# Kernel optimization log

Hardware: AMD Instinct MI355X
Metric: run time of the kernel (lower is better)

The kernel has to match this reference:

```python
import jax, jax.numpy as jnp
import numpy as np

NJ, NS, NM, NR = 100000, 20000, 10000, 5000
D_IN, OUT, H = 128, 256, 4
C = OUT // H
E = 250000
NEG_SLOPE = 0.2
LN_EPS = 1e-5


def setup_inputs() -> dict:
    key = jax.random.key(0)
    ks = jax.random.split(key, 24)
    inp = {
        'x_job':     jax.random.normal(ks[0], (NJ, D_IN), jnp.float32),
        'x_station': jax.random.normal(ks[1], (NS, D_IN), jnp.float32),
        'x_machine': jax.random.normal(ks[2], (NM, D_IN), jnp.float32),
        'x_robot':   jax.random.normal(ks[3], (NR, D_IN), jnp.float32),
        'src_cl': jax.random.randint(ks[4],  (E,), 0, NS, jnp.int32),
        'dst_cl': jax.random.randint(ks[5],  (E,), 0, NJ, jnp.int32),
        'src_ld': jax.random.randint(ks[6],  (E,), 0, NS, jnp.int32),
        'dst_ld': jax.random.randint(ks[7],  (E,), 0, NJ, jnp.int32),
        'src_we': jax.random.randint(ks[8],  (E,), 0, NM, jnp.int32),
        'dst_we': jax.random.randint(ks[9],  (E,), 0, NJ, jnp.int32),
        'src_ex': jax.random.randint(ks[10], (E,), 0, NM, jnp.int32),
        'dst_ex': jax.random.randint(ks[11], (E,), 0, NJ, jnp.int32),
        'src_hd': jax.random.randint(ks[12], (E,), 0, NR, jnp.int32),
        'dst_hd': jax.random.randint(ks[13], (E,), 0, NJ, jnp.int32),
        'Ws':      jax.random.normal(ks[14], (5, D_IN, OUT), jnp.float32) * 0.05,
        'att_src': jax.random.normal(ks[15], (5, H, C), jnp.float32) * 0.05,
        'att_dst': jax.random.normal(ks[16], (5, H, C), jnp.float32) * 0.05,
        'biases':  jnp.zeros((5, OUT), jnp.float32),
        'W_res':   jax.random.normal(ks[17], (D_IN, OUT), jnp.float32) * 0.05,
        'ln_gamma': jnp.ones((OUT,), jnp.float32),
        'ln_beta':  jnp.zeros((OUT,), jnp.float32),
    }
    return inp


def _gat(x_src, x_dst, src, dst, W, a_src, a_dst, b):
    # Bipartite GATConv (PyG semantics, shared lin for src and dst, concat heads)
    hs = (x_src @ W).reshape(-1, H, C)   # [Ns,H,C]
    hd = (x_dst @ W).reshape(-1, H, C)   # [Nd,H,C]
    a_s = jnp.einsum('nhc,hc->nh', hs, a_src)  # [Ns,H]
    a_d = jnp.einsum('nhc,hc->nh', hd, a_dst)  # [Nd,H]
    e = jax.nn.leaky_relu(a_s[src] + a_d[dst], NEG_SLOPE)  # [E,H]
    # softmax over incoming edges of each dst node
    m = jax.ops.segment_max(e, dst, num_segments=NJ)       # [Nd,H]
    ex = jnp.exp(e - m[dst])
    denom = jax.ops.segment_sum(ex, dst, num_segments=NJ)
    alpha = ex / (denom[dst] + 1e-16)                       # [E,H]
    msg = alpha[:, :, None] * hs[src]                        # [E,H,C]
    out = jax.ops.segment_sum(msg, dst, num_segments=NJ)    # [Nd,H,C]
    return out.reshape(NJ, H * C) + b


def reference(x_job, x_station, x_machine, x_robot,
              src_cl, dst_cl, src_ld, dst_ld, src_we, dst_we,
              src_ex, dst_ex, src_hd, dst_hd,
              Ws, att_src, att_dst, biases, W_res, ln_gamma, ln_beta):
    rels = [
        (x_station, src_cl, dst_cl),
        (x_station, src_ld, dst_ld),
        (x_machine, src_we, dst_we),
        (x_machine, src_ex, dst_ex),
        (x_robot,   src_hd, dst_hd),
    ]
    acc = jnp.zeros((NJ, OUT), x_job.dtype)
    for i, (xs, s, d) in enumerate(rels):  # sum aggregation across relations
        acc = acc + _gat(xs, x_job, s, d, Ws[i], att_src[i], att_dst[i], biases[i])
    h = acc + x_job @ W_res                # residual projection (dj != out_dim)
    h = jax.nn.relu(h)
    mu = jnp.mean(h, axis=-1, keepdims=True)
    var = jnp.var(h, axis=-1, keepdims=True)
    return (h - mu) * jax.lax.rsqrt(var + LN_EPS) * ln_gamma + ln_beta
```

## Files before the change

kernel.cpp:

```cpp
#include <hip/hip_runtime.h>

typedef unsigned short u16;
typedef unsigned int u32;
typedef __attribute__((ext_vector_type(8))) short s16x8;
typedef __attribute__((ext_vector_type(4))) float f32x4;

__device__ __forceinline__ float bf2f(u16 u) { return __uint_as_float(((u32)u) << 16); }
__device__ __forceinline__ u16 f2bf(float f) {
    u32 b = __float_as_uint(f);
    b += 0x7fffu + ((b >> 16) & 1u);
    return (u16)(b >> 16);
}

__global__ void probe_mark(float* __restrict__ out, int n, float val) {
    int i = blockIdx.x * blockDim.x + threadIdx.x;
    if (i < n) out[i] = val;
}

struct PrepX { const float* x[4]; int rows[4]; int blks[4]; u16* xb[4]; };

__global__ void k_prep_all(const float* __restrict__ Ws, const float* __restrict__ W_res,
                           const float* __restrict__ att_src, const float* __restrict__ att_dst,
                           const float* __restrict__ biases,
                           u32* __restrict__ cnt, int zc, int nzb, u16* __restrict__ wt,
                           float* __restrict__ w_d_all, float* __restrict__ w_s_cat,
                           float* __restrict__ bias_sum, PrepX PX) {
    int b = blockIdx.x;
    if (b < nzb) {
        int i = b * 256 + threadIdx.x;
        if (i < zc) cnt[i] = 0u;
        return;
    }
    b -= nzb;
    if (b < 768) {
        int i = b * 256 + threadIdx.x;
        int k = i & 127;
        int c = (i >> 7) & 255;
        int w = i >> 15;
        float v = (w < 5) ? Ws[(size_t)w * 32768 + k * 256 + c] : W_res[k * 256 + c];
        wt[i] = f2bf(v);
        return;
    }
    b -= 768;
    if (b < 6) {
        if (b < 5) {
            int k = threadIdx.x;
            if (k >= 128) return;
            const float* Wr = Ws + (size_t)b * 128 * 256 + (size_t)k * 256;
            for (int h = 0; h < 4; ++h) {
                float ss = 0.f, sd = 0.f;
                for (int c = 0; c < 64; ++c) {
                    float w = Wr[h * 64 + c];
                    ss += w * att_src[(b * 4 + h) * 64 + c];
                    sd += w * att_dst[(b * 4 + h) * 64 + c];
                }
                w_d_all[k * 20 + b * 4 + h] = sd;
                w_s_cat[b * 512 + k * 4 + h] = ss;
            }
        } else if (threadIdx.x < 256) {
            float s = 0.f;
            for (int r = 0; r < 5; ++r) s += biases[r * 256 + threadIdx.x];
            bias_sum[threadIdx.x] = s;
        }
        return;
    }
    b -= 6;
#pragma unroll
    for (int a = 0; a < 4; ++a) {
        if (b < PX.blks[a]) {
            int elem = b * 2048 + threadIdx.x * 8;
            if (elem < PX.rows[a] * 128) {
                const float4* src = (const float4*)(PX.x[a] + elem);
                float4 v0 = src[0], v1 = src[1];
                u32 w0 = ((u32)f2bf(v0.y) << 16) | f2bf(v0.x);
                u32 w1 = ((u32)f2bf(v0.w) << 16) | f2bf(v0.z);
                u32 w2 = ((u32)f2bf(v1.y) << 16) | f2bf(v1.x);
                u32 w3 = ((u32)f2bf(v1.w) << 16) | f2bf(v1.z);
                *(uint4*)(PX.xb[a] + elem) = make_uint4(w0, w1, w2, w3);
            }
            return;
        }
        b -= PX.blks[a];
    }
}

struct SDesc { const float* A; const float* W; float* out; int N; int Kout; int groups; int start; };
struct STab { SDesc d[6]; int total; };

__global__ void skinny_all(STab T) {
    int idx = blockIdx.x * blockDim.x + threadIdx.x;
    if (idx >= T.total) return;
    int mi = 0;
#pragma unroll
    for (int i = 1; i < 6; ++i) if (idx >= T.d[i].start) mi = i;
    SDesc d = T.d[mi];
    int local = idx - d.start;
    int row = local / d.groups, g = local - row * d.groups;
    const float* a = d.A + (size_t)row * 128;
    const float* w = d.W + g * 4;
    int Kout = d.Kout;
    float s0 = 0.f, s1 = 0.f, s2 = 0.f, s3 = 0.f;
    for (int k = 0; k < 128; k += 4) {
        float4 av = *(const float4*)(a + k);
        float4 w0 = *(const float4*)(w + (size_t)(k + 0) * Kout);
        float4 w1 = *(const float4*)(w + (size_t)(k + 1) * Kout);
        float4 w2 = *(const float4*)(w + (size_t)(k + 2) * Kout);
        float4 w3 = *(const float4*)(w + (size_t)(k + 3) * Kout);
        s0 += av.x * w0.x + av.y * w1.x + av.z * w2.x + av.w * w3.x;
        s1 += av.x * w0.y + av.y * w1.y + av.z * w2.y + av.w * w3.y;
        s2 += av.x * w0.z + av.y * w1.z + av.z * w2.z + av.w * w3.z;
        s3 += av.x * w0.w + av.y * w1.w + av.z * w2.w + av.w * w3.w;
    }
    float* o = d.out + (size_t)row * Kout + g * 4;
    *(float4*)o = make_float4(s0, s1, s2, s3);
}

struct GDesc { const u16* A; u16* C; int wslice; int N; int start; };
struct GTab { GDesc d[6]; };

__global__ __launch_bounds__(256) void gemm_all(GTab T, const u16* __restrict__ wt) {
    __shared__ __align__(16) u16 sA[64][136];
    __shared__ __align__(16) u16 sB[64][136];
    int bx = blockIdx.x;
    int mi = 0;
#pragma unroll
    for (int i = 1; i < 6; ++i) if (bx >= T.d[i].start) mi = i;
    GDesc d = T.d[mi];
    int R0 = (bx - d.start) * 64;
    int t = threadIdx.x;
    int r = t >> 2, seg = (t & 3) * 32;
    {
        uint4 a0, a1, a2, a3;
        if (R0 + r < d.N) {
            const uint4* pa = (const uint4*)(d.A + (size_t)(R0 + r) * 128 + seg);
            a0 = pa[0]; a1 = pa[1]; a2 = pa[2]; a3 = pa[3];
        } else {
            a0 = a1 = a2 = a3 = make_uint4(0, 0, 0, 0);
        }
        uint4* qd = (uint4*)&sA[r][seg];
        qd[0] = a0; qd[1] = a1; qd[2] = a2; qd[3] = a3;
    }
    int wave = t >> 6, lane = t & 63;
    int quad = lane >> 4, m = lane & 15;
    const u16* aRow = &sA[wave * 16 + m][0];
    const u16* wbase = wt + (size_t)d.wslice * 32768;

    for (int y = 0; y < 4; ++y) {
        int c0 = y * 64;
        const uint4* pb = (const uint4*)(wbase + (size_t)(c0 + r) * 128 + seg);
        uint4 b0 = pb[0], b1 = pb[1], b2 = pb[2], b3 = pb[3];
        __syncthreads();
        uint4* qb = (uint4*)&sB[r][seg];
        qb[0] = b0; qb[1] = b1; qb[2] = b2; qb[3] = b3;
        __syncthreads();

        f32x4 acc[4] = {};
#pragma unroll
        for (int k0 = 0; k0 < 128; k0 += 32) {
            s16x8 af = *(const s16x8*)(aRow + k0 + quad * 8);
#pragma unroll
            for (int ct = 0; ct < 4; ++ct) {
                s16x8 bf = *(const s16x8*)(&sB[ct * 16 + m][k0 + quad * 8]);
                acc[ct] = __builtin_amdgcn_mfma_f32_16x16x32_bf16(af, bf, acc[ct], 0, 0, 0);
            }
        }
#pragma unroll
        for (int ct = 0; ct < 4; ++ct) {
#pragma unroll
            for (int i = 0; i < 4; ++i) {
                int row = R0 + wave * 16 + quad * 4 + i;
                if (row < d.N) d.C[(size_t)row * 256 + c0 + ct * 16 + m] = f2bf(acc[ct][i]);
            }
        }
    }
}

struct EdgeP { const int* src[5]; const int* dst[5]; int base[5]; };

__global__ void k_count(EdgeP P, u32* __restrict__ cnt, u32* __restrict__ epos, int E) {
    int r = blockIdx.y;
    int e = blockIdx.x * blockDim.x + threadIdx.x;
    if (e >= E) return;
    u32 c = atomicAdd(cnt + (size_t)P.dst[r][e] * 5 + r, 1u);
    epos[(size_t)r * E + e] = c;
}

__global__ void k_scan1(const u32* __restrict__ cnt, u32* __restrict__ off,
                        u32* __restrict__ bsum, int nblk) {
    int b = blockIdx.x, t = threadIdx.x;
    size_t base = (size_t)b * 1024 + t * 4;
    u32 v0 = cnt[base], v1 = cnt[base + 1], v2 = cnt[base + 2], v3 = cnt[base + 3];
    u32 tsum = v0 + v1 + v2 + v3;
    __shared__ u32 s[256];
    u32 x = tsum;
    s[t] = x; __syncthreads();
    for (int ofs = 1; ofs < 256; ofs <<= 1) {
        u32 y = (t >= ofs) ? s[t - ofs] : 0u;
        __syncthreads();
        x += y; s[t] = x;
        __syncthreads();
    }
    u32 ex = x - tsum;
    off[base] = ex; off[base + 1] = ex + v0; off[base + 2] = ex + v0 + v1; off[base + 3] = ex + v0 + v1 + v2;
    if (t == 255) bsum[b] = x;
}

__global__ void k_scan23(u32* __restrict__ off, const u32* __restrict__ bsum, int nblk) {
    int b = blockIdx.x, t = threadIdx.x;
    __shared__ u32 s[256];
    u32 part = 0;
    for (int i = t; i < b; i += 256) part += bsum[i];
    s[t] = part; __syncthreads();
    for (int ofs = 128; ofs; ofs >>= 1) {
        if (t < ofs) s[t] += s[t + ofs];
        __syncthreads();
    }
    u32 add = s[0];
    size_t base = (size_t)b * 1024 + t * 4;
    off[base] += add; off[base + 1] += add; off[base + 2] += add; off[base + 3] += add;
}

__global__ void k_fill(EdgeP P, const u32* __restrict__ off, const u32* __restrict__ epos,
                       u32* __restrict__ epay, int E) {
    int r = blockIdx.y;
    int e = blockIdx.x * blockDim.x + threadIdx.x;
    if (e >= E) return;
    int d = P.dst[r][e];
    u32 pos = off[(size_t)d * 5 + r] + epos[(size_t)r * E + e];
    epay[pos] = (u32)(P.base[r] + P.src[r][e]);
}

__global__ __launch_bounds__(512) void k_gather(
        const u32* __restrict__ offs, const u32* __restrict__ epay,
        const float* __restrict__ as_h,
        const float* __restrict__ a_d,
        const u16* __restrict__ hs, const u16* __restrict__ resb,
        const float* __restrict__ bias_sum,
        const float* __restrict__ gamma, const float* __restrict__ beta,
        float* __restrict__ out, int NJ) {
    int row = blockIdx.x * 8 + (threadIdx.x >> 6);
    int lane = threadIdx.x & 63;
    if (row >= NJ) return;

    ushort4 rr = *(const ushort4*)(resb + (size_t)row * 256 + lane * 4);
    float4 bb = *(const float4*)(bias_sum + lane * 4);
    int c = lane * 4;
    float4 g = *(const float4*)(gamma + c);
    float4 be = *(const float4*)(beta + c);

    int hd = lane >> 4;
    u32 hoff = (u32)(lane << 2);

    const float* adb = a_d + (size_t)row * 20 + hd;
    float adx[5] = { adb[0], adb[4], adb[8], adb[12], adb[16] };

    const u32* op = offs + (size_t)row * 5;
    u32 o[6];
#pragma unroll
    for (int i = 0; i < 6; ++i) o[i] = op[i];
    u32 deg = o[5] - o[0];

    u32 pv = 0;
    if (deg) {
        u32 li = (u32)lane < deg ? (u32)lane : 0u;
        pv = epay[o[0] + li];
    }

    float a0 = 0.f, a1 = 0.f, a2 = 0.f, a3 = 0.f;
#pragma unroll
    for (int r = 0; r < 5; ++r) {
        float adr = adx[r];
        float n0 = 0.f, n1 = 0.f, n2 = 0.f, n3 = 0.f, dsum = 0.f;
        for (u32 e = o[r]; e < o[r + 1]; ++e) {
            u32 i = e - o[0];
            u32 p;
            if (i < 64u) p = __shfl(pv, (int)i);
            else         p = epay[e];
            float x = as_h[p * 4 + (u32)hd] + adr;
            x = x > 0.f ? x : 0.2f * x;
            float w = __expf(x);
            dsum += w;
            ushort4 hv = *(const ushort4*)(hs + ((size_t)p << 8) + hoff);
            n0 += w * bf2f(hv.x); n1 += w * bf2f(hv.y);
            n2 += w * bf2f(hv.z); n3 += w * bf2f(hv.w);
        }
        float iv = 1.f / (dsum + 1e-16f);
        a0 += n0 * iv; a1 += n1 * iv; a2 += n2 * iv; a3 += n3 * iv;
    }

    float h0 = fmaxf(a0 + bf2f(rr.x) + bb.x, 0.f);
    float h1 = fmaxf(a1 + bf2f(rr.y) + bb.y, 0.f);
    float h2 = fmaxf(a2 + bf2f(rr.z) + bb.z, 0.f);
    float h3 = fmaxf(a3 + bf2f(rr.w) + bb.w, 0.f);
    float s = h0 + h1 + h2 + h3;
    float s2 = h0 * h0 + h1 * h1 + h2 * h2 + h3 * h3;
    for (int o2 = 32; o2; o2 >>= 1) {
        s += __shfl_xor(s, o2);
        s2 += __shfl_xor(s2, o2);
    }
    float mu = s * (1.f / 256.f);
    float var = s2 * (1.f / 256.f) - mu * mu;
    float rs = rsqrtf(var + 1e-5f);
    float4 o4;
    o4.x = (h0 - mu) * rs * g.x + be.x;
    o4.y = (h1 - mu) * rs * g.y + be.y;
    o4.z = (h2 - mu) * rs * g.z + be.z;
    o4.w = (h3 - mu) * rs * g.w + be.w;
    *(float4*)(out + (size_t)row * 256 + c) = o4;
}

static size_t align256(size_t x) { return (x + 255) & ~(size_t)255; }

extern "C" void kernel_launch(void* const* d_in, const int* in_sizes, int n_in,
                              void* d_out, int out_size, void* d_ws, size_t ws_size,
                              hipStream_t stream) {
    float* out = (float*)d_out;

    int NJ = in_sizes[0] / 128, NS = in_sizes[1] / 128, NM = in_sizes[2] / 128, NR = in_sizes[3] / 128;
    int E = in_sizes[4];
    bool cfg_ok = (n_in >= 21) && (out_size == NJ * 256)
        && (in_sizes[14] == 5 * 128 * 256) && (in_sizes[18] == 128 * 256)
        && (in_sizes[19] == 256) && (in_sizes[20] == 256);
    if (!cfg_ok) { probe_mark<<<8, 256, 0, stream>>>(out, 2048, 1000000.0f); return; }

    const float* x_job = (const float*)d_in[0];
    const float* x_st  = (const float*)d_in[1];
    const float* x_ma  = (const float*)d_in[2];
    const float* x_ro  = (const float*)d_in[3];
    EdgeP EP;
    EP.src[0] = (const int*)d_in[4];  EP.dst[0] = (const int*)d_in[5];
    EP.src[1] = (const int*)d_in[6];  EP.dst[1] = (const int*)d_in[7];
    EP.src[2] = (const int*)d_in[8];  EP.dst[2] = (const int*)d_in[9];
    EP.src[3] = (const int*)d_in[10]; EP.dst[3] = (const int*)d_in[11];
    EP.src[4] = (const int*)d_in[12]; EP.dst[4] = (const int*)d_in[13];
    EP.base[0] = 0; EP.base[1] = NS; EP.base[2] = 2 * NS;
    EP.base[3] = 2 * NS + NM; EP.base[4] = 2 * NS + 2 * NM;
    const float* Ws      = (const float*)d_in[14];
    const float* att_src = (const float*)d_in[15];
    const float* att_dst = (const float*)d_in[16];
    const float* biases  = (const float*)d_in[17];
    const float* W_res   = (const float*)d_in[18];
    const float* gamma   = (const float*)d_in[19];
    const float* beta    = (const float*)d_in[20];

    int nseg = 5 * NJ;
    int nblk = (nseg + 1023) / 1024;
    int NPAD = nblk * 1024;
    int TOT = 2 * NS + 2 * NM + NR;
    int TOTX = NJ + NS + NM + NR;

    char* base = (char*)d_ws;
    size_t ob = 0;
    float*  w_d_all  = (float*)(base + ob);  ob += align256(128 * 20 * 4);
    float*  w_s_cat  = (float*)(base + ob);  ob += align256(5 * 128 * 4 * 4);
    float*  bias_sum = (float*)(base + ob);  ob += align256(256 * 4);
    float*  a_d      = (float*)(base + ob);  ob += align256((size_t)NJ * 20 * 4);
    float*  as_cat   = (float*)(base + ob);  ob += align256((size_t)TOT * 4 * 4);
    u16*    wt       = (u16*)(base + ob);    ob += align256((size_t)6 * 256 * 128 * 2);
    u16*    xb       = (u16*)(base + ob);    ob += align256((size_t)TOTX * 128 * 2);
    u16*    resb     = (u16*)(base + ob);    ob += align256((size_t)NJ * 256 * 2);
    u16*    hs_cat   = (u16*)(base + ob);    ob += align256((size_t)TOT * 256 * 2);
    u32*    cnt      = (u32*)(base + ob);    ob += align256((size_t)NPAD * 4);
    u32*    offs     = (u32*)(base + ob);    ob += align256((size_t)NPAD * 4);
    u32*    bsum     = (u32*)(base + ob);    ob += align256((size_t)nblk * 4);
    u32*    epos     = (u32*)(base + ob);    ob += align256((size_t)5 * E * 4);
    u32*    epay     = (u32*)(base + ob);    ob += align256((size_t)5 * E * 4);

    if (ws_size < ob) { probe_mark<<<8, 256, 0, stream>>>(out, 2048, 500000.0f); return; }

    int zc = NPAD;
    int nzb = (zc + 255) / 256;
    PrepX PX;
    PX.x[0] = x_job; PX.x[1] = x_st; PX.x[2] = x_ma; PX.x[3] = x_ro;
    PX.rows[0] = NJ; PX.rows[1] = NS; PX.rows[2] = NM; PX.rows[3] = NR;
    u16* xb_job = xb;
    u16* xb_st  = xb + (size_t)NJ * 128;
    u16* xb_ma  = xb + (size_t)(NJ + NS) * 128;
    u16* xb_ro  = xb + (size_t)(NJ + NS + NM) * 128;
    PX.xb[0] = xb_job; PX.xb[1] = xb_st; PX.xb[2] = xb_ma; PX.xb[3] = xb_ro;
    int nxb = 0;
    for (int a = 0; a < 4; ++a) { PX.blks[a] = (PX.rows[a] * 128 + 2047) / 2048; nxb += PX.blks[a]; }
    k_prep_all<<<nzb + 768 + 6 + nxb, 256, 0, stream>>>(Ws, W_res, att_src, att_dst, biases,
                                                        cnt, zc, nzb, wt,
                                                        w_d_all, w_s_cat, bias_sum, PX);

    STab ST;
    int st = 0;
    ST.d[0] = {x_job, w_d_all,           a_d,                             NJ, 20, 5, st}; st += NJ * 5;
    ST.d[1] = {x_st,  w_s_cat + 0 * 512, as_cat + (size_t)EP.base[0] * 4, NS, 4, 1, st}; st += NS;
    ST.d[2] = {x_st,  w_s_cat + 1 * 512, as_cat + (size_t)EP.base[1] * 4, NS, 4, 1, st}; st += NS;
    ST.d[3] = {x_ma,  w_s_cat + 2 * 512, as_cat + (size_t)EP.base[2] * 4, NM, 4, 1, st}; st += NM;
    ST.d[4] = {x_ma,  w_s_cat + 3 * 512, as_cat + (size_t)EP.base[3] * 4, NM, 4, 1, st}; st += NM;
    ST.d[5] = {x_ro,  w_s_cat + 4 * 512, as_cat + (size_t)EP.base[4] * 4, NR, 4, 1, st}; st += NR;
    ST.total = st;
    skinny_all<<<(ST.total + 255) / 256, 256, 0, stream>>>(ST);

    int tJ = (NJ + 63) / 64, tS = (NS + 63) / 64, tM = (NM + 63) / 64, tR = (NR + 63) / 64;
    GTab GT;
    int gs = 0;
    GT.d[0] = {xb_job, resb,                              5, NJ, gs}; gs += tJ;
    GT.d[1] = {xb_st,  hs_cat + (size_t)EP.base[0] * 256, 0, NS, gs}; gs += tS;
    GT.d[2] = {xb_st,  hs_cat + (size_t)EP.base[1] * 256, 1, NS, gs}; gs += tS;
    GT.d[3] = {xb_ma,  hs_cat + (size_t)EP.base[2] * 256, 2, NM, gs}; gs += tM;
    GT.d[4] = {xb_ma,  hs_cat + (size_t)EP.base[3] * 256, 3, NM, gs}; gs += tM;
    GT.d[5] = {xb_ro,  hs_cat + (size_t)EP.base[4] * 256, 4, NR, gs}; gs += tR;
    gemm_all<<<gs, 256, 0, stream>>>(GT, wt);

    k_count<<<dim3((E + 255) / 256, 5), 256, 0, stream>>>(EP, cnt, epos, E);
    k_scan1<<<nblk, 256, 0, stream>>>(cnt, offs, bsum, nblk);
    k_scan23<<<nblk, 256, 0, stream>>>(offs, bsum, nblk);
    k_fill<<<dim3((E + 255) / 256, 5), 256, 0, stream>>>(EP, offs, epos, epay, E);

    k_gather<<<(NJ + 7) / 8, 512, 0, stream>>>(offs, epay, as_cat,
                                               a_d, hs_cat, resb, bias_sum,
                                               gamma, beta, out, NJ);
}
```

Baseline: 529.0 us.

## Merge GEMM, skinny projection and edge-count kernels into one interleaved launch

```diff
diff --git a/kernel.cpp b/kernel.cpp
--- a/kernel.cpp
+++ b/kernel.cpp
@@ -2,6 +2,7 @@
 
 typedef unsigned short u16;
 typedef unsigned int u32;
+typedef unsigned long long u64;
 typedef __attribute__((ext_vector_type(8))) short s16x8;
 typedef __attribute__((ext_vector_type(4))) float f32x4;
 
@@ -86,103 +87,109 @@
 
 struct SDesc { const float* A; const float* W; float* out; int N; int Kout; int groups; int start; };
 struct STab { SDesc d[6]; int total; };
-
-__global__ void skinny_all(STab T) {
-    int idx = blockIdx.x * blockDim.x + threadIdx.x;
-    if (idx >= T.total) return;
-    int mi = 0;
-#pragma unroll
-    for (int i = 1; i < 6; ++i) if (idx >= T.d[i].start) mi = i;
-    SDesc d = T.d[mi];
-    int local = idx - d.start;
-    int row = local / d.groups, g = local - row * d.groups;
-    const float* a = d.A + (size_t)row * 128;
-    const float* w = d.W + g * 4;
-    int Kout = d.Kout;
-    float s0 = 0.f, s1 = 0.f, s2 = 0.f, s3 = 0.f;
-    for (int k = 0; k < 128; k += 4) {
-        float4 av = *(const float4*)(a + k);
-        float4 w0 = *(const float4*)(w + (size_t)(k + 0) * Kout);
-        float4 w1 = *(const float4*)(w + (size_t)(k + 1) * Kout);
-        float4 w2 = *(const float4*)(w + (size_t)(k + 2) * Kout);
-        float4 w3 = *(const float4*)(w + (size_t)(k + 3) * Kout);
-        s0 += av.x * w0.x + av.y * w1.x + av.z * w2.x + av.w * w3.x;
-        s1 += av.x * w0.y + av.y * w1.y + av.z * w2.y + av.w * w3.y;
-        s2 += av.x * w0.z + av.y * w1.z + av.z * w2.z + av.w * w3.z;
-        s3 += av.x * w0.w + av.y * w1.w + av.z * w2.w + av.w * w3.w;
-    }
-    float* o = d.out + (size_t)row * Kout + g * 4;
-    *(float4*)o = make_float4(s0, s1, s2, s3);
-}
-
 struct GDesc { const u16* A; u16* C; int wslice; int N; int start; };
 struct GTab { GDesc d[6]; };
-
-__global__ __launch_bounds__(256) void gemm_all(GTab T, const u16* __restrict__ wt) {
+struct EdgeP { const int* src[5]; const int* dst[5]; int base[5]; };
+
+__global__ __launch_bounds__(256) void k_mid(GTab T, const u16* __restrict__ wt,
+                                             STab S, EdgeP P,
+                                             u32* __restrict__ cnt, u32* __restrict__ epos,
+                                             int E, int nEB, int G, int C, int SB) {
     __shared__ __align__(16) u16 sA[64][136];
     __shared__ __align__(16) u16 sB[64][136];
-    int bx = blockIdx.x;
-    int mi = 0;
-#pragma unroll
-    for (int i = 1; i < 6; ++i) if (bx >= T.d[i].start) mi = i;
-    GDesc d = T.d[mi];
-    int R0 = (bx - d.start) * 64;
+    int q = blockIdx.x / 11, p = blockIdx.x % 11;
     int t = threadIdx.x;
-    int r = t >> 2, seg = (t & 3) * 32;
-    {
-        uint4 a0, a1, a2, a3;
-        if (R0 + r < d.N) {
-            const uint4* pa = (const uint4*)(d.A + (size_t)(R0 + r) * 128 + seg);
-            a0 = pa[0]; a1 = pa[1]; a2 = pa[2]; a3 = pa[3];
-        } else {
-            a0 = a1 = a2 = a3 = make_uint4(0, 0, 0, 0);
-        }
-        uint4* qd = (uint4*)&sA[r][seg];
-        qd[0] = a0; qd[1] = a1; qd[2] = a2; qd[3] = a3;
-    }
-    int wave = t >> 6, lane = t & 63;
-    int quad = lane >> 4, m = lane & 15;
-    const u16* aRow = &sA[wave * 16 + m][0];
-    const u16* wbase = wt + (size_t)d.wslice * 32768;
-
-    for (int y = 0; y < 4; ++y) {
-        int c0 = y * 64;
-        const uint4* pb = (const uint4*)(wbase + (size_t)(c0 + r) * 128 + seg);
-        uint4 b0 = pb[0], b1 = pb[1], b2 = pb[2], b3 = pb[3];
-        __syncthreads();
-        uint4* qb = (uint4*)&sB[r][seg];
-        qb[0] = b0; qb[1] = b1; qb[2] = b2; qb[3] = b3;
-        __syncthreads();
-
-        f32x4 acc[4] = {};
-#pragma unroll
-        for (int k0 = 0; k0 < 128; k0 += 32) {
-            s16x8 af = *(const s16x8*)(aRow + k0 + quad * 8);
+
+    if (p < 3) {
+        int bx = q * 3 + p;
+        if (bx >= G) return;
+        int mi = 0;
+#pragma unroll
+        for (int i = 1; i < 6; ++i) if (bx >= T.d[i].start) mi = i;
+        GDesc d = T.d[mi];
+        int R0 = (bx - d.start) * 64;
+        int r = t >> 2, seg = (t & 3) * 32;
+        {
+            uint4 a0, a1, a2, a3;
+            if (R0 + r < d.N) {
+                const uint4* pa = (const uint4*)(d.A + (size_t)(R0 + r) * 128 + seg);
+                a0 = pa[0]; a1 = pa[1]; a2 = pa[2]; a3 = pa[3];
+            } else {
+                a0 = a1 = a2 = a3 = make_uint4(0, 0, 0, 0);
+            }
+            uint4* qd = (uint4*)&sA[r][seg];
+            qd[0] = a0; qd[1] = a1; qd[2] = a2; qd[3] = a3;
+        }
+        int wave = t >> 6, lane = t & 63;
+        int quad = lane >> 4, m = lane & 15;
+        const u16* aRow = &sA[wave * 16 + m][0];
+        const u16* wbase = wt + (size_t)d.wslice * 32768;
+
+        for (int y = 0; y < 4; ++y) {
+            int c0 = y * 64;
+            const uint4* pb = (const uint4*)(wbase + (size_t)(c0 + r) * 128 + seg);
+            uint4 b0 = pb[0], b1 = pb[1], b2 = pb[2], b3 = pb[3];
+            __syncthreads();
+            uint4* qb = (uint4*)&sB[r][seg];
+            qb[0] = b0; qb[1] = b1; qb[2] = b2; qb[3] = b3;
+            __syncthreads();
+
+            f32x4 acc[4] = {};
+#pragma unroll
+            for (int k0 = 0; k0 < 128; k0 += 32) {
+                s16x8 af = *(const s16x8*)(aRow + k0 + quad * 8);
+#pragma unroll
+                for (int ct = 0; ct < 4; ++ct) {
+                    s16x8 bf = *(const s16x8*)(&sB[ct * 16 + m][k0 + quad * 8]);
+                    acc[ct] = __builtin_amdgcn_mfma_f32_16x16x32_bf16(af, bf, acc[ct], 0, 0, 0);
+                }
+            }
 #pragma unroll
             for (int ct = 0; ct < 4; ++ct) {
-                s16x8 bf = *(const s16x8*)(&sB[ct * 16 + m][k0 + quad * 8]);
-                acc[ct] = __builtin_amdgcn_mfma_f32_16x16x32_bf16(af, bf, acc[ct], 0, 0, 0);
+#pragma unroll
+                for (int i = 0; i < 4; ++i) {
+                    int row = R0 + wave * 16 + quad * 4 + i;
+                    if (row < d.N) d.C[(size_t)row * 256 + c0 + ct * 16 + m] = f2bf(acc[ct][i]);
+                }
             }
         }
-#pragma unroll
-        for (int ct = 0; ct < 4; ++ct) {
-#pragma unroll
-            for (int i = 0; i < 4; ++i) {
-                int row = R0 + wave * 16 + quad * 4 + i;
-                if (row < d.N) d.C[(size_t)row * 256 + c0 + ct * 16 + m] = f2bf(acc[ct][i]);
-            }
-        }
-    }
-}
-
-struct EdgeP { const int* src[5]; const int* dst[5]; int base[5]; };
-
-__global__ void k_count(EdgeP P, u32* __restrict__ cnt, u32* __restrict__ epos, int E) {
-    int r = blockIdx.y;
-    int e = blockIdx.x * blockDim.x + threadIdx.x;
-    if (e >= E) return;
-    u32 c = atomicAdd(cnt + (size_t)P.dst[r][e] * 5 + r, 1u);
-    epos[(size_t)r * E + e] = c;
+    } else if (p < 8) {
+        int i = q * 5 + (p - 3);
+        if (i >= C) return;
+        int r = i / nEB, eb = i - r * nEB;
+        int e = eb * 256 + t;
+        if (e >= E) return;
+        u32 c = atomicAdd(cnt + (size_t)P.dst[r][e] * 5 + r, 1u);
+        epos[(size_t)r * E + e] = c;
+    } else {
+        int i = q * 3 + (p - 8);
+        if (i >= SB) return;
+        int idx = i * 256 + t;
+        if (idx >= S.total) return;
+        int mi = 0;
+#pragma unroll
+        for (int j = 1; j < 6; ++j) if (idx >= S.d[j].start) mi = j;
+        SDesc d = S.d[mi];
+        int local = idx - d.start;
+        int row = local / d.groups, g = local - row * d.groups;
+        const float* a = d.A + (size_t)row * 128;
+        const float* w = d.W + g * 4;
+        int Kout = d.Kout;
+        float s0 = 0.f, s1 = 0.f, s2 = 0.f, s3 = 0.f;
+        for (int k = 0; k < 128; k += 4) {
+            float4 av = *(const float4*)(a + k);
+            float4 w0 = *(const float4*)(w + (size_t)(k + 0) * Kout);
+            float4 w1 = *(const float4*)(w + (size_t)(k + 1) * Kout);
+            float4 w2 = *(const float4*)(w + (size_t)(k + 2) * Kout);
+            float4 w3 = *(const float4*)(w + (size_t)(k + 3) * Kout);
+            s0 += av.x * w0.x + av.y * w1.x + av.z * w2.x + av.w * w3.x;
+            s1 += av.x * w0.y + av.y * w1.y + av.z * w2.y + av.w * w3.y;
+            s2 += av.x * w0.z + av.y * w1.z + av.z * w2.z + av.w * w3.z;
+            s3 += av.x * w0.w + av.y * w1.w + av.z * w2.w + av.w * w3.w;
+        }
+        float* o = d.out + (size_t)row * Kout + g * 4;
+        *(float4*)o = make_float4(s0, s1, s2, s3);
+    }
 }
 
 __global__ void k_scan1(const u32* __restrict__ cnt, u32* __restrict__ off,
@@ -393,7 +400,6 @@
     ST.d[4] = {x_ma,  w_s_cat + 3 * 512, as_cat + (size_t)EP.base[3] * 4, NM, 4, 1, st}; st += NM;
     ST.d[5] = {x_ro,  w_s_cat + 4 * 512, as_cat + (size_t)EP.base[4] * 4, NR, 4, 1, st}; st += NR;
     ST.total = st;
-    skinny_all<<<(ST.total + 255) / 256, 256, 0, stream>>>(ST);
 
     int tJ = (NJ + 63) / 64, tS = (NS + 63) / 64, tM = (NM + 63) / 64, tR = (NR + 63) / 64;
     GTab GT;
@@ -404,12 +410,17 @@
     GT.d[3] = {xb_ma,  hs_cat + (size_t)EP.base[2] * 256, 2, NM, gs}; gs += tM;
     GT.d[4] = {xb_ma,  hs_cat + (size_t)EP.base[3] * 256, 3, NM, gs}; gs += tM;
     GT.d[5] = {xb_ro,  hs_cat + (size_t)EP.base[4] * 256, 4, NR, gs}; gs += tR;
-    gemm_all<<<gs, 256, 0, stream>>>(GT, wt);
-
-    k_count<<<dim3((E + 255) / 256, 5), 256, 0, stream>>>(EP, cnt, epos, E);
+
+    int nEB = (E + 255) / 256;
+    int G = gs, C = 5 * nEB, SB = (ST.total + 255) / 256;
+    int stripes = (G + 2) / 3;
+    if ((C + 4) / 5 > stripes) stripes = (C + 4) / 5;
+    if ((SB + 2) / 3 > stripes) stripes = (SB + 2) / 3;
+    k_mid<<<stripes * 11, 256, 0, stream>>>(GT, wt, ST, EP, cnt, epos, E, nEB, G, C, SB);
+
     k_scan1<<<nblk, 256, 0, stream>>>(cnt, offs, bsum, nblk);
     k_scan23<<<nblk, 256, 0, stream>>>(offs, bsum, nblk);
-    k_fill<<<dim3((E + 255) / 256, 5), 256, 0, stream>>>(EP, offs, epos, epay, E);
+    k_fill<<<dim3(nEB, 5), 256, 0, stream>>>(EP, offs, epos, epay, E);
 
     k_gather<<<(NJ + 7) / 8, 512, 0, stream>>>(offs, epay, as_cat,
                                                a_d, hs_cat, resb, bias_sum,
```

Measured after the change: 490.0 us. 7.4% less time.
